# Performance work log

Measured on AMD Instinct MI355X. Metric: run time of the kernel, lower is better.

## Reference

```python
import jax, jax.numpy as jnp
import numpy as np


def _conv1x1(x, w, b):
    # x: (b, c_in, t, h, w); w: (c_out, c_in); b: (c_out,)
    return jnp.einsum('bcthw,oc->bothw', x, w) + b[None, :, None, None, None]


def _maxpool_hw(x):
    # MaxPool3d(kernel=(1,2,2)): pool spatial dims by 2 (h, w assumed even)
    b, c, t, h, w = x.shape
    return x.reshape(b, c, t, h // 2, 2, w // 2, 2).max(axis=(4, 6))


def setup_inputs() -> dict:
    key = jax.random.key(0)
    ks = jax.random.split(key, 9)
    C, CI = 256, 128  # in_channels, inter_channels = in_channels // 2
    B, T, H, W = 8, 8, 28, 28
    s = 1.0 / np.sqrt(C)
    si = 1.0 / np.sqrt(CI)
    return {
        'x': jax.random.normal(ks[0], (B, C, T, H, W), jnp.float32),
        'g_w': jax.random.normal(ks[1], (CI, C), jnp.float32) * s,
        'g_b': jax.random.normal(ks[2], (CI,), jnp.float32) * 0.01,
        'theta_w': jax.random.normal(ks[3], (CI, C), jnp.float32) * s,
        'theta_b': jax.random.normal(ks[4], (CI,), jnp.float32) * 0.01,
        'phi_w': jax.random.normal(ks[5], (CI, C), jnp.float32) * s,
        'phi_b': jax.random.normal(ks[6], (CI,), jnp.float32) * 0.01,
        'W_w': jax.random.normal(ks[7], (C, CI), jnp.float32) * si,
        'W_b': jax.random.normal(ks[8], (C,), jnp.float32) * 0.01,
    }


def reference(x, g_w, g_b, theta_w, theta_b, phi_w, phi_b, W_w, W_b):
    b, c, t, h, w = x.shape
    ci = g_w.shape[0]
    # g and phi paths are sub-sampled by MaxPool3d(1,2,2)
    g_x = _maxpool_hw(_conv1x1(x, g_w, g_b)).reshape(b, ci, -1)          # (b, ci, M)
    g_x = g_x.transpose(0, 2, 1)                                          # (b, M, ci)
    theta_x = _conv1x1(x, theta_w, theta_b).reshape(b, ci, -1)            # (b, ci, N)
    theta_x = theta_x.transpose(0, 2, 1)                                  # (b, N, ci)
    phi_x = _maxpool_hw(_conv1x1(x, phi_w, phi_b)).reshape(b, ci, -1)     # (b, ci, M)
    f = jnp.einsum('bnc,bcm->bnm', theta_x, phi_x)                        # (b, N, M)
    f_div_C = jax.nn.softmax(f, axis=-1)
    y = jnp.einsum('bnm,bmc->bnc', f_div_C, g_x)                          # (b, N, ci)
    y = y.transpose(0, 2, 1).reshape(b, ci, t, h, w)
    W_y = _conv1x1(y, W_w, W_b)
    return W_y + x
```

## Files before the change

kernel.cpp:

```cpp
#include <hip/hip_runtime.h>

typedef _Float16 f16;
typedef f16 half8 __attribute__((ext_vector_type(8)));
typedef float f32x4 __attribute__((ext_vector_type(4)));

#define MFMA16(a, b, c) __builtin_amdgcn_mfma_f32_16x16x32_f16((a), (b), (c), 0, 0, 0)

static constexpr int B = 8, C = 256, CI = 128, N = 6272, M = 1568, MP = 1600;

static constexpr size_t oXT = 0;
static constexpr size_t oQ  = (size_t)B * N * C;
static constexpr size_t oPF = oQ  + (size_t)B * N * CI;
static constexpr size_t oGF = oPF + (size_t)B * N * CI;
static constexpr size_t oPP = oGF + (size_t)B * N * CI;
static constexpr size_t oGT = oPP + (size_t)B * MP * CI;
static constexpr size_t oW  = oGT + (size_t)B * MP * CI;

static __device__ __forceinline__ half8 hmax8(half8 a, half8 b) {
    half8 r;
#pragma unroll
    for (int j = 0; j < 8; j++) r[j] = a[j] > b[j] ? a[j] : b[j];
    return r;
}

static __device__ __forceinline__ float rowmax16(float x) {
    int t;
    t = __builtin_amdgcn_update_dpp(__float_as_int(x), __float_as_int(x), 0x121, 0xF, 0xF, false);
    x = fmaxf(x, __int_as_float(t));
    t = __builtin_amdgcn_update_dpp(__float_as_int(x), __float_as_int(x), 0x122, 0xF, 0xF, false);
    x = fmaxf(x, __int_as_float(t));
    t = __builtin_amdgcn_update_dpp(__float_as_int(x), __float_as_int(x), 0x124, 0xF, 0xF, false);
    x = fmaxf(x, __int_as_float(t));
    t = __builtin_amdgcn_update_dpp(__float_as_int(x), __float_as_int(x), 0x128, 0xF, 0xF, false);
    x = fmaxf(x, __int_as_float(t));
    return x;
}

__global__ void k_prep(const float* tw, const float* pw, const float* gw,
                       const float* Ww, f16* dst) {
    int i = blockIdx.x * 256 + threadIdx.x;
    int s = i >> 15, j = i & 32767;
    float v;
    if (s == 0) v = tw[j];
    else if (s == 1) v = pw[j];
    else if (s == 2) v = gw[j];
    else v = Ww[j];
    dst[i] = (f16)v;
}

__global__ void k_trans(const float* x, f16* xT) {
    __shared__ float tile[32][33];
    int b = blockIdx.z, nt = blockIdx.x, ct = blockIdx.y;
    int tx = threadIdx.x, ty = threadIdx.y;
#pragma unroll
    for (int i = 0; i < 4; i++) {
        int c = ct * 32 + ty + i * 8;
        tile[ty + i * 8][tx] = x[(size_t)(b * C + c) * N + nt * 32 + tx];
    }
    __syncthreads();
#pragma unroll
    for (int i = 0; i < 4; i++) {
        int n = nt * 32 + ty + i * 8;
        xT[(size_t)(b * N + n) * C + ct * 32 + tx] = (f16)tile[tx][ty + i * 8];
    }
}

__global__ __launch_bounds__(256) void k_proj(const f16* __restrict__ xT,
                                              const f16* __restrict__ w16,
                                              const float* __restrict__ bias,
                                              f16* __restrict__ out) {
    __shared__ f16 xs[128 * 72];
    __shared__ f16 ws[128 * 72];
    int b = blockIdx.z, n0 = blockIdx.x * 128;
    int tid = threadIdx.x, w = tid >> 6, lane = tid & 63, ln = lane & 15, quad = lane >> 4;
    f32x4 acc[2][8];
#pragma unroll
    for (int rb = 0; rb < 2; rb++)
#pragma unroll
        for (int cb = 0; cb < 8; cb++) acc[rb][cb] = (f32x4){0.f, 0.f, 0.f, 0.f};

    for (int kc = 0; kc < 4; kc++) {
#pragma unroll
        for (int i = 0; i < 4; i++) {
            int qq = tid + i * 256;
            int row = qq >> 3, coff = (qq & 7) * 8;
            *(int4*)&xs[row * 72 + coff] =
                *(const int4*)&xT[(size_t)(b * N + n0 + row) * C + kc * 64 + coff];
            *(int4*)&ws[row * 72 + coff] =
                *(const int4*)&w16[(size_t)row * C + kc * 64 + coff];
        }
        __syncthreads();
#pragma unroll
        for (int ks = 0; ks < 2; ks++) {
            half8 a0 = *(const half8*)&xs[(w * 32 + ln) * 72 + ks * 32 + quad * 8];
            half8 a1 = *(const half8*)&xs[(w * 32 + 16 + ln) * 72 + ks * 32 + quad * 8];
#pragma unroll
            for (int cb = 0; cb < 8; cb++) {
                half8 bf = *(const half8*)&ws[(cb * 16 + ln) * 72 + ks * 32 + quad * 8];
                acc[0][cb] = MFMA16(a0, bf, acc[0][cb]);
                acc[1][cb] = MFMA16(a1, bf, acc[1][cb]);
            }
        }
        __syncthreads();
    }
#pragma unroll
    for (int cb = 0; cb < 8; cb++) {
        float bv = bias[cb * 16 + ln];
#pragma unroll
        for (int rb = 0; rb < 2; rb++) {
#pragma unroll
            for (int r = 0; r < 4; r++) {
                int n = n0 + w * 32 + rb * 16 + quad * 4 + r;
                out[(size_t)(b * N + n) * CI + cb * 16 + ln] = (f16)(acc[rb][cb][r] + bv);
            }
        }
    }
}

__global__ __launch_bounds__(256) void k_pool(const f16* __restrict__ phiF, const f16* __restrict__ gF,
                                              f16* __restrict__ phiP, f16* __restrict__ gPT) {
    __shared__ f16 gt[128 * 72];
    int b = blockIdx.y, mt = blockIdx.x;
    int tid = threadIdx.x;
#pragma unroll
    for (int i = 0; i < 4; i++) {
        int qq = tid + i * 256;
        int ml = qq >> 4, coff = (qq & 15) * 8;
        int m = mt * 64 + ml;
        half8 pv, gv;
        if (m < M) {
            int t = m / 196, rr = m % 196, hp = rr / 14, wp = rr % 14;
            int nb = t * 784 + hp * 56 + wp * 2;
            size_t base = ((size_t)(b * N) + nb) * CI + coff;
            half8 p0 = *(const half8*)&phiF[base];
            half8 p1 = *(const half8*)&phiF[base + CI];
            half8 p2 = *(const half8*)&phiF[base + 28 * CI];
            half8 p3 = *(const half8*)&phiF[base + 29 * CI];
            pv = hmax8(hmax8(p0, p1), hmax8(p2, p3));
            half8 g0 = *(const half8*)&gF[base];
            half8 g1 = *(const half8*)&gF[base + CI];
            half8 g2 = *(const half8*)&gF[base + 28 * CI];
            half8 g3 = *(const half8*)&gF[base + 29 * CI];
            gv = hmax8(hmax8(g0, g1), hmax8(g2, g3));
        } else {
#pragma unroll
            for (int j = 0; j < 8; j++) { pv[j] = (f16)0.f; gv[j] = (f16)0.f; }
        }
        *(half8*)&phiP[((size_t)b * MP + m) * CI + coff] = pv;
#pragma unroll
        for (int j = 0; j < 8; j++) gt[(coff + j) * 72 + ml] = gv[j];
    }
    __syncthreads();
#pragma unroll
    for (int i = 0; i < 4; i++) {
        int qq = tid + i * 256;
        int ci = qq >> 3, moff = (qq & 7) * 8;
        *(int4*)&gPT[((size_t)(b * CI) + ci) * MP + mt * 64 + moff] = *(const int4*)&gt[ci * 72 + moff];
    }
}

__global__ __launch_bounds__(256, 2) void k_attn(const f16* __restrict__ q,
                                                 const f16* __restrict__ kk,
                                                 const f16* __restrict__ v,
                                                 f16* __restrict__ y) {
    __shared__ f16 Ks[64 * 136];
    __shared__ f16 Vs[128 * 72];
    __shared__ f16 Ps[4 * 32 * 72];
    int b = blockIdx.y, n0 = blockIdx.x * 128;
    int tid = threadIdx.x, w = tid >> 6, lane = tid & 63, ln = lane & 15, quad = lane >> 4;
    int wq = n0 + w * 32;
    f16* Pw = &Ps[w * 32 * 72];

    half8 qf[2][4];
#pragma unroll
    for (int qt = 0; qt < 2; qt++)
#pragma unroll
        for (int ks = 0; ks < 4; ks++) {
            qf[qt][ks] = *(const half8*)&q[(size_t)(b * N + wq + qt * 16 + ln) * CI + ks * 32 + quad * 8];
#pragma unroll
            for (int j = 0; j < 8; j++) qf[qt][ks][j] *= (f16)1.4426950408889634f;
        }

    f32x4 O[2][8], Osum[2];
#pragma unroll
    for (int qt = 0; qt < 2; qt++) {
        Osum[qt] = (f32x4){0.f, 0.f, 0.f, 0.f};
#pragma unroll
        for (int cb = 0; cb < 8; cb++) O[qt][cb] = (f32x4){0.f, 0.f, 0.f, 0.f};
    }
    float mi[2][4] = {{-1e30f, -1e30f, -1e30f, -1e30f}, {-1e30f, -1e30f, -1e30f, -1e30f}};

    for (int mc = 0; mc < 25; mc++) {
#pragma unroll
        for (int i = 0; i < 4; i++) {
            int qq = tid + i * 256;
            int kr = qq >> 4, kc = (qq & 15) * 8;
            *(int4*)&Ks[kr * 136 + kc] = *(const int4*)&kk[((size_t)b * MP + mc * 64 + kr) * CI + kc];
            int vr = qq >> 3, vc = (qq & 7) * 8;
            *(int4*)&Vs[vr * 72 + vc] = *(const int4*)&v[((size_t)(b * CI) + vr) * MP + mc * 64 + vc];
        }
        __syncthreads();

        f32x4 S[2][4];
#pragma unroll
        for (int mt = 0; mt < 4; mt++) {
            f32x4 s0 = (f32x4){0.f, 0.f, 0.f, 0.f}, s1 = (f32x4){0.f, 0.f, 0.f, 0.f};
#pragma unroll
            for (int ks = 0; ks < 4; ks++) {
                half8 kb = *(const half8*)&Ks[(mt * 16 + ln) * 136 + ks * 32 + quad * 8];
                s0 = MFMA16(qf[0][ks], kb, s0);
                s1 = MFMA16(qf[1][ks], kb, s1);
            }
            S[0][mt] = s0; S[1][mt] = s1;
        }

#pragma unroll
        for (int qt = 0; qt < 2; qt++)
#pragma unroll
            for (int r = 0; r < 4; r++) {
                float vm = fmaxf(fmaxf(S[qt][0][r], S[qt][1][r]), fmaxf(S[qt][2][r], S[qt][3][r]));
                vm = rowmax16(vm);
                float mnew = fmaxf(mi[qt][r], vm);
                float alpha = __builtin_amdgcn_exp2f(mi[qt][r] - mnew);
                mi[qt][r] = mnew;
#pragma unroll
                for (int mt = 0; mt < 4; mt++) {
                    float p = __builtin_amdgcn_exp2f(S[qt][mt][r] - mnew);
                    Pw[(qt * 16 + quad * 4 + r) * 72 + mt * 16 + ln] = (f16)p;
                }
#pragma unroll
                for (int cb = 0; cb < 8; cb++) O[qt][cb][r] *= alpha;
                Osum[qt][r] *= alpha;
            }

#pragma unroll
        for (int ks = 0; ks < 2; ks++) {
            half8 a0 = *(const half8*)&Pw[ln * 72 + ks * 32 + quad * 8];
            half8 a1 = *(const half8*)&Pw[(16 + ln) * 72 + ks * 32 + quad * 8];
            f16 ov = (mc * 64 + ks * 32 < M) ? (f16)1.0f : (f16)0.0f;
            half8 on;
#pragma unroll
            for (int j = 0; j < 8; j++) on[j] = ov;
#pragma unroll
            for (int cb = 0; cb < 8; cb++) {
                half8 bv = *(const half8*)&Vs[(cb * 16 + ln) * 72 + ks * 32 + quad * 8];
                O[0][cb] = MFMA16(a0, bv, O[0][cb]);
                O[1][cb] = MFMA16(a1, bv, O[1][cb]);
            }
            Osum[0] = MFMA16(a0, on, Osum[0]);
            Osum[1] = MFMA16(a1, on, Osum[1]);
        }
        __syncthreads();
    }

#pragma unroll
    for (int qt = 0; qt < 2; qt++)
#pragma unroll
        for (int cb = 0; cb < 8; cb++)
#pragma unroll
            for (int r = 0; r < 4; r++) {
                int n = wq + qt * 16 + quad * 4 + r;
                y[(size_t)(b * N + n) * CI + cb * 16 + ln] = (f16)(O[qt][cb][r] / Osum[qt][r]);
            }
}

__global__ __launch_bounds__(256) void k_final(const f16* __restrict__ y,
                                               const f16* __restrict__ Ww,
                                               const float* __restrict__ Wb,
                                               const float* __restrict__ x,
                                               float* __restrict__ out) {
    __shared__ f16 ys[64 * 136];
    __shared__ f16 Ws[128 * 136];
    int b = blockIdx.z, ch = blockIdx.y, n0 = blockIdx.x * 64;
    int tid = threadIdx.x, w = tid >> 6, lane = tid & 63, ln = lane & 15, quad = lane >> 4;
#pragma unroll
    for (int i = 0; i < 4; i++) {
        int qq = tid + i * 256; int row = qq >> 4, coff = (qq & 15) * 8;
        *(int4*)&ys[row * 136 + coff] =
            *(const int4*)&y[(size_t)(b * N + n0 + row) * CI + coff];
    }
#pragma unroll
    for (int i = 0; i < 8; i++) {
        int qq = tid + i * 256; int row = qq >> 4, coff = (qq & 15) * 8;
        *(int4*)&Ws[row * 136 + coff] =
            *(const int4*)&Ww[(size_t)(ch * 128 + row) * CI + coff];
    }
    __syncthreads();
    f32x4 acc[2][4];
#pragma unroll
    for (int rb = 0; rb < 2; rb++)
#pragma unroll
        for (int nb = 0; nb < 4; nb++) acc[rb][nb] = (f32x4){0.f, 0.f, 0.f, 0.f};
#pragma unroll
    for (int ks = 0; ks < 4; ks++) {
        half8 a0 = *(const half8*)&Ws[(w * 32 + ln) * 136 + ks * 32 + quad * 8];
        half8 a1 = *(const half8*)&Ws[(w * 32 + 16 + ln) * 136 + ks * 32 + quad * 8];
#pragma unroll
        for (int nb = 0; nb < 4; nb++) {
            half8 bf = *(const half8*)&ys[(nb * 16 + ln) * 136 + ks * 32 + quad * 8];
            acc[0][nb] = MFMA16(a0, bf, acc[0][nb]);
            acc[1][nb] = MFMA16(a1, bf, acc[1][nb]);
        }
    }
#pragma unroll
    for (int rb = 0; rb < 2; rb++) {
        int cbase = ch * 128 + w * 32 + rb * 16 + quad * 4;
#pragma unroll
        for (int nb = 0; nb < 4; nb++) {
#pragma unroll
            for (int r = 0; r < 4; r++) {
                int c = cbase + r;
                size_t addr = (size_t)(b * C + c) * N + n0 + nb * 16 + ln;
                out[addr] = acc[rb][nb][r] + Wb[c] + x[addr];
            }
        }
    }
}

extern "C" void kernel_launch(void* const* d_in, const int* in_sizes, int n_in,
                              void* d_out, int out_size, void* d_ws, size_t ws_size,
                              hipStream_t stream) {
    const float* x  = (const float*)d_in[0];
    const float* gw = (const float*)d_in[1];
    const float* gb = (const float*)d_in[2];
    const float* tw = (const float*)d_in[3];
    const float* tb = (const float*)d_in[4];
    const float* pw = (const float*)d_in[5];
    const float* pb = (const float*)d_in[6];
    const float* Ww = (const float*)d_in[7];
    const float* Wb = (const float*)d_in[8];
    float* out = (float*)d_out;
    f16* ws = (f16*)d_ws;

    f16* xT   = ws + oXT;
    f16* Q    = ws + oQ;
    f16* phiF = ws + oPF;
    f16* gF   = ws + oGF;
    f16* phiP = ws + oPP;
    f16* gPT  = ws + oGT;
    f16* Y    = ws + oPF;
    f16* w16  = ws + oW;

    k_prep<<<512, 256, 0, stream>>>(tw, pw, gw, Ww, w16);
    k_trans<<<dim3(196, 8, 8), dim3(32, 8), 0, stream>>>(x, xT);
    k_proj<<<dim3(49, 1, 8), 256, 0, stream>>>(xT, w16,         tb, Q);
    k_proj<<<dim3(49, 1, 8), 256, 0, stream>>>(xT, w16 + 32768, pb, phiF);
    k_proj<<<dim3(49, 1, 8), 256, 0, stream>>>(xT, w16 + 65536, gb, gF);
    k_pool<<<dim3(25, 8), 256, 0, stream>>>(phiF, gF, phiP, gPT);
    k_attn<<<dim3(49, 8), 256, 0, stream>>>(Q, phiP, gPT, Y);
    k_final<<<dim3(98, 2, 8), 256, 0, stream>>>(Y, w16 + 98304, Wb, x, out);
    (void)in_sizes; (void)n_in; (void)out_size; (void)ws_size;
}
```

Baseline: 268.6 us.

## Prefetch attention K/V tiles in registers, halve query tile, lazy rescale

Result: slower. 422.3 us (+57.2%).

```diff
diff --git a/kernel.cpp b/kernel.cpp
--- a/kernel.cpp
+++ b/kernel.cpp
@@ -50,7 +50,7 @@
 
 __global__ void k_trans(const float* x, f16* xT) {
     __shared__ float tile[32][33];
-    int b = blockIdx.z, nt = blockIdx.x, ct = blockIdx.y;
+    int b = blockIdx.x, nt = blockIdx.y, ct = blockIdx.z;
     int tx = threadIdx.x, ty = threadIdx.y;
 #pragma unroll
     for (int i = 0; i < 4; i++) {
@@ -71,7 +71,7 @@
                                               f16* __restrict__ out) {
     __shared__ f16 xs[128 * 72];
     __shared__ f16 ws[128 * 72];
-    int b = blockIdx.z, n0 = blockIdx.x * 128;
+    int b = blockIdx.x, n0 = blockIdx.y * 128;
     int tid = threadIdx.x, w = tid >> 6, lane = tid & 63, ln = lane & 15, quad = lane >> 4;
     f32x4 acc[2][8];
 #pragma unroll
@@ -120,7 +120,7 @@
 __global__ __launch_bounds__(256) void k_pool(const f16* __restrict__ phiF, const f16* __restrict__ gF,
                                               f16* __restrict__ phiP, f16* __restrict__ gPT) {
     __shared__ f16 gt[128 * 72];
-    int b = blockIdx.y, mt = blockIdx.x;
+    int b = blockIdx.x, mt = blockIdx.y;
     int tid = threadIdx.x;
 #pragma unroll
     for (int i = 0; i < 4; i++) {
@@ -159,84 +159,96 @@
     }
 }
 
-__global__ __launch_bounds__(256, 2) void k_attn(const f16* __restrict__ q,
+__global__ __launch_bounds__(256, 3) void k_attn(const f16* __restrict__ q,
                                                  const f16* __restrict__ kk,
                                                  const f16* __restrict__ v,
                                                  f16* __restrict__ y) {
     __shared__ f16 Ks[64 * 136];
     __shared__ f16 Vs[128 * 72];
-    __shared__ f16 Ps[4 * 32 * 72];
-    int b = blockIdx.y, n0 = blockIdx.x * 128;
+    __shared__ f16 Ps[4 * 16 * 72];
+    int b = blockIdx.x, n0 = blockIdx.y * 64;
     int tid = threadIdx.x, w = tid >> 6, lane = tid & 63, ln = lane & 15, quad = lane >> 4;
-    int wq = n0 + w * 32;
-    f16* Pw = &Ps[w * 32 * 72];
-
-    half8 qf[2][4];
-#pragma unroll
-    for (int qt = 0; qt < 2; qt++)
-#pragma unroll
-        for (int ks = 0; ks < 4; ks++) {
-            qf[qt][ks] = *(const half8*)&q[(size_t)(b * N + wq + qt * 16 + ln) * CI + ks * 32 + quad * 8];
-#pragma unroll
-            for (int j = 0; j < 8; j++) qf[qt][ks][j] *= (f16)1.4426950408889634f;
-        }
-
-    f32x4 O[2][8], Osum[2];
-#pragma unroll
-    for (int qt = 0; qt < 2; qt++) {
-        Osum[qt] = (f32x4){0.f, 0.f, 0.f, 0.f};
-#pragma unroll
-        for (int cb = 0; cb < 8; cb++) O[qt][cb] = (f32x4){0.f, 0.f, 0.f, 0.f};
-    }
-    float mi[2][4] = {{-1e30f, -1e30f, -1e30f, -1e30f}, {-1e30f, -1e30f, -1e30f, -1e30f}};
+    int wq = n0 + w * 16;
+    f16* Pw = &Ps[w * 16 * 72];
+
+    int kr = tid >> 4, kc = (tid & 15) * 8;
+    int vr = tid >> 3, vc = (tid & 7) * 8;
+    const f16* kbase = kk + ((size_t)b * MP + kr) * CI + kc;
+    const f16* vbase = v + ((size_t)(b * CI) + vr) * MP + vc;
+
+    int4 kpf[4], vpf[4];
+#pragma unroll
+    for (int i = 0; i < 4; i++) {
+        kpf[i] = *(const int4*)(kbase + (size_t)i * 16 * CI);
+        vpf[i] = *(const int4*)(vbase + (size_t)i * 32 * MP);
+    }
+
+    half8 qf[4];
+#pragma unroll
+    for (int ks = 0; ks < 4; ks++) {
+        qf[ks] = *(const half8*)&q[(size_t)(b * N + wq + ln) * CI + ks * 32 + quad * 8];
+#pragma unroll
+        for (int j = 0; j < 8; j++) qf[ks][j] *= (f16)1.4426950408889634f;
+    }
+
+    f32x4 O[8], Osum = (f32x4){0.f, 0.f, 0.f, 0.f};
+#pragma unroll
+    for (int cb = 0; cb < 8; cb++) O[cb] = (f32x4){0.f, 0.f, 0.f, 0.f};
+    float mi[4] = {-1e30f, -1e30f, -1e30f, -1e30f};
 
     for (int mc = 0; mc < 25; mc++) {
+        __syncthreads();
 #pragma unroll
         for (int i = 0; i < 4; i++) {
-            int qq = tid + i * 256;
-            int kr = qq >> 4, kc = (qq & 15) * 8;
-            *(int4*)&Ks[kr * 136 + kc] = *(const int4*)&kk[((size_t)b * MP + mc * 64 + kr) * CI + kc];
-            int vr = qq >> 3, vc = (qq & 7) * 8;
-            *(int4*)&Vs[vr * 72 + vc] = *(const int4*)&v[((size_t)(b * CI) + vr) * MP + mc * 64 + vc];
+            *(int4*)&Ks[(kr + i * 16) * 136 + kc] = kpf[i];
+            *(int4*)&Vs[(vr + i * 32) * 72 + vc] = vpf[i];
         }
         __syncthreads();
-
-        f32x4 S[2][4];
+        if (mc < 24) {
+#pragma unroll
+            for (int i = 0; i < 4; i++) {
+                kpf[i] = *(const int4*)(kbase + ((size_t)(mc + 1) * 64 + (size_t)i * 16) * CI);
+                vpf[i] = *(const int4*)(vbase + (size_t)(mc + 1) * 64 + (size_t)i * 32 * MP);
+            }
+        }
+
+        f32x4 S[4];
+        __builtin_amdgcn_s_setprio(1);
 #pragma unroll
         for (int mt = 0; mt < 4; mt++) {
-            f32x4 s0 = (f32x4){0.f, 0.f, 0.f, 0.f}, s1 = (f32x4){0.f, 0.f, 0.f, 0.f};
+            f32x4 s = (f32x4){0.f, 0.f, 0.f, 0.f};
 #pragma unroll
             for (int ks = 0; ks < 4; ks++) {
                 half8 kb = *(const half8*)&Ks[(mt * 16 + ln) * 136 + ks * 32 + quad * 8];
-                s0 = MFMA16(qf[0][ks], kb, s0);
-                s1 = MFMA16(qf[1][ks], kb, s1);
-            }
-            S[0][mt] = s0; S[1][mt] = s1;
-        }
-
-#pragma unroll
-        for (int qt = 0; qt < 2; qt++)
-#pragma unroll
-            for (int r = 0; r < 4; r++) {
-                float vm = fmaxf(fmaxf(S[qt][0][r], S[qt][1][r]), fmaxf(S[qt][2][r], S[qt][3][r]));
-                vm = rowmax16(vm);
-                float mnew = fmaxf(mi[qt][r], vm);
-                float alpha = __builtin_amdgcn_exp2f(mi[qt][r] - mnew);
-                mi[qt][r] = mnew;
-#pragma unroll
-                for (int mt = 0; mt < 4; mt++) {
-                    float p = __builtin_amdgcn_exp2f(S[qt][mt][r] - mnew);
-                    Pw[(qt * 16 + quad * 4 + r) * 72 + mt * 16 + ln] = (f16)p;
-                }
-#pragma unroll
-                for (int cb = 0; cb < 8; cb++) O[qt][cb][r] *= alpha;
-                Osum[qt][r] *= alpha;
-            }
-
+                s = MFMA16(qf[ks], kb, s);
+            }
+            S[mt] = s;
+        }
+        __builtin_amdgcn_s_setprio(0);
+
+#pragma unroll
+        for (int r = 0; r < 4; r++) {
+            float vm = fmaxf(fmaxf(S[0][r], S[1][r]), fmaxf(S[2][r], S[3][r]));
+            vm = rowmax16(vm);
+            if (__ballot(vm > mi[r] + 8.f)) {
+                float mnew = fmaxf(mi[r], vm);
+                float alpha = __builtin_amdgcn_exp2f(mi[r] - mnew);
+                mi[r] = mnew;
+#pragma unroll
+                for (int cb = 0; cb < 8; cb++) O[cb][r] *= alpha;
+                Osum[r] *= alpha;
+            }
+#pragma unroll
+            for (int mt = 0; mt < 4; mt++) {
+                float p = __builtin_amdgcn_exp2f(S[mt][r] - mi[r]);
+                Pw[(quad * 4 + r) * 72 + mt * 16 + ln] = (f16)p;
+            }
+        }
+
+        __builtin_amdgcn_s_setprio(1);
 #pragma unroll
         for (int ks = 0; ks < 2; ks++) {
-            half8 a0 = *(const half8*)&Pw[ln * 72 + ks * 32 + quad * 8];
-            half8 a1 = *(const half8*)&Pw[(16 + ln) * 72 + ks * 32 + quad * 8];
+            half8 a = *(const half8*)&Pw[ln * 72 + ks * 32 + quad * 8];
             f16 ov = (mc * 64 + ks * 32 < M) ? (f16)1.0f : (f16)0.0f;
             half8 on;
 #pragma unroll
@@ -244,24 +256,20 @@
 #pragma unroll
             for (int cb = 0; cb < 8; cb++) {
                 half8 bv = *(const half8*)&Vs[(cb * 16 + ln) * 72 + ks * 32 + quad * 8];
-                O[0][cb] = MFMA16(a0, bv, O[0][cb]);
-                O[1][cb] = MFMA16(a1, bv, O[1][cb]);
-            }
-            Osum[0] = MFMA16(a0, on, Osum[0]);
-            Osum[1] = MFMA16(a1, on, Osum[1]);
-        }
-        __syncthreads();
-    }
-
-#pragma unroll
-    for (int qt = 0; qt < 2; qt++)
-#pragma unroll
-        for (int cb = 0; cb < 8; cb++)
-#pragma unroll
-            for (int r = 0; r < 4; r++) {
-                int n = wq + qt * 16 + quad * 4 + r;
-                y[(size_t)(b * N + n) * CI + cb * 16 + ln] = (f16)(O[qt][cb][r] / Osum[qt][r]);
-            }
+                O[cb] = MFMA16(a, bv, O[cb]);
+            }
+            Osum = MFMA16(a, on, Osum);
+        }
+        __builtin_amdgcn_s_setprio(0);
+    }
+
+#pragma unroll
+    for (int cb = 0; cb < 8; cb++)
+#pragma unroll
+        for (int r = 0; r < 4; r++) {
+            int n = wq + quad * 4 + r;
+            y[(size_t)(b * N + n) * CI + cb * 16 + ln] = (f16)(O[cb][r] / Osum[r]);
+        }
 }
 
 __global__ __launch_bounds__(256) void k_final(const f16* __restrict__ y,
@@ -271,7 +279,7 @@
                                                float* __restrict__ out) {
     __shared__ f16 ys[64 * 136];
     __shared__ f16 Ws[128 * 136];
-    int b = blockIdx.z, ch = blockIdx.y, n0 = blockIdx.x * 64;
+    int b = blockIdx.x, ch = blockIdx.z, n0 = blockIdx.y * 64;
     int tid = threadIdx.x, w = tid >> 6, lane = tid & 63, ln = lane & 15, quad = lane >> 4;
 #pragma unroll
     for (int i = 0; i < 4; i++) {
@@ -342,12 +350,12 @@
     f16* w16  = ws + oW;
 
     k_prep<<<512, 256, 0, stream>>>(tw, pw, gw, Ww, w16);
-    k_trans<<<dim3(196, 8, 8), dim3(32, 8), 0, stream>>>(x, xT);
-    k_proj<<<dim3(49, 1, 8), 256, 0, stream>>>(xT, w16,         tb, Q);
-    k_proj<<<dim3(49, 1, 8), 256, 0, stream>>>(xT, w16 + 32768, pb, phiF);
-    k_proj<<<dim3(49, 1, 8), 256, 0, stream>>>(xT, w16 + 65536, gb, gF);
-    k_pool<<<dim3(25, 8), 256, 0, stream>>>(phiF, gF, phiP, gPT);
-    k_attn<<<dim3(49, 8), 256, 0, stream>>>(Q, phiP, gPT, Y);
-    k_final<<<dim3(98, 2, 8), 256, 0, stream>>>(Y, w16 + 98304, Wb, x, out);
+    k_trans<<<dim3(8, 196, 8), dim3(32, 8), 0, stream>>>(x, xT);
+    k_proj<<<dim3(8, 49), 256, 0, stream>>>(xT, w16,         tb, Q);
+    k_proj<<<dim3(8, 49), 256, 0, stream>>>(xT, w16 + 32768, pb, phiF);
+    k_proj<<<dim3(8, 49), 256, 0, stream>>>(xT, w16 + 65536, gb, gF);
+    k_pool<<<dim3(8, 25), 256, 0, stream>>>(phiF, gF, phiP, gPT);
+    k_attn<<<dim3(8, 98), 256, 0, stream>>>(Q, phiP, gPT, Y);
+    k_final<<<dim3(8, 98, 2), 256, 0, stream>>>(Y, w16 + 98304, Wb, x, out);
     (void)in_sizes; (void)n_in; (void)out_size; (void)ws_size;
 }
```
